# Optimization experiments

Hardware: AMD Instinct MI355X
Metric: run time of the kernel (lower is better)

## Reference

```python
import jax, jax.numpy as jnp
import numpy as np

D, H, W = 256, 256, 256
R = 6                      # max_radius: per-Gaussian half-window in voxels


def setup_inputs() -> dict:
    key = jax.random.key(0)
    k1, k2, k3, k4, k5 = jax.random.split(key, 5)
    N = 20000
    center_vox = jax.random.uniform(k1, (N, 3), minval=float(R), maxval=float(D - R), dtype=jnp.float32)
    A = jax.random.normal(k2, (N, 3, 3), dtype=jnp.float32) * 0.5
    # SPD inverse covariance in normalized coords (diffs divided by half_shape ~128)
    cov_inv = (jnp.einsum('nij,nkj->nik', A, A) + jnp.eye(3, dtype=jnp.float32)) * 2000.0
    density_r = jax.random.normal(k3, (N,), dtype=jnp.float32)
    density_i = jax.random.normal(k4, (N,), dtype=jnp.float32)
    radius_vox = jax.random.uniform(k5, (N,), minval=3.0, maxval=float(R), dtype=jnp.float32)
    half_shape = jnp.array([D / 2.0, H / 2.0, W / 2.0], dtype=jnp.float32)
    return {
        'center_vox': center_vox,
        'cov_inv': cov_inv,
        'density_r': density_r,
        'density_i': density_i,
        'radius_vox': radius_vox,
        'half_shape': half_shape,
    }


def reference(center_vox, cov_inv, density_r, density_i, radius_vox, half_shape):
    # Per-Gaussian fixed window of side (2R+1); gather -> Mahalanobis weight -> scatter-add.
    offs = jnp.arange(-R, R + 1, dtype=jnp.int32)
    od, oh, ow = jnp.meshgrid(offs, offs, offs, indexing='ij')
    off = jnp.stack([od, oh, ow], axis=-1).reshape(-1, 3)          # [K3,3]
    base = jnp.floor(center_vox).astype(jnp.int32)                  # [N,3]
    vox = base[:, None, :] + off[None, :, :]                        # [N,K3,3] int
    voxf = vox.astype(center_vox.dtype)
    diff = (voxf - center_vox[:, None, :]) / half_shape             # normalized diff [N,K3,3]
    Md = jnp.einsum('nkd,nde,nke->nk', diff, cov_inv, diff)         # Mahalanobis [N,K3]
    # bbox mask (floor(c-r) .. ceil(c+r)) as in build_tile_pairs / CUDA kernel
    bmin = jnp.floor(center_vox - radius_vox[:, None])
    bmax = jnp.ceil(center_vox + radius_vox[:, None])
    in_bbox = jnp.all((voxf >= bmin[:, None, :]) & (voxf <= bmax[:, None, :]), axis=-1)
    dims = jnp.array([D, H, W], dtype=jnp.int32)
    in_grid = jnp.all((vox >= 0) & (vox < dims), axis=-1)
    mask = (Md <= 9.0) & in_bbox & in_grid
    w = jnp.exp(-0.5 * Md) * mask.astype(Md.dtype)                  # [N,K3]
    flat = jnp.where(in_grid, vox[..., 0] * (H * W) + vox[..., 1] * W + vox[..., 2], 0).reshape(-1)
    vol_r = jnp.zeros(D * H * W, dtype=w.dtype).at[flat].add((w * density_r[:, None]).reshape(-1))
    vol_i = jnp.zeros(D * H * W, dtype=w.dtype).at[flat].add((w * density_i[:, None]).reshape(-1))
    return vol_r.reshape(D, H, W), vol_i.reshape(D, H, W)
```

## Files before the change

kernel.cpp:

```cpp
#include <hip/hip_runtime.h>

#define DD 256
#define HH 256
#define WW 256
#define RMAX 6

#define NTX 64
#define NTY 64
#define NTZ 16
#define NTILES (NTX * NTY * NTZ)
#define CAP 32
#define OVF_CAP 8192

__global__ __launch_bounds__(256) void fill_kernel(
    const float* __restrict__ center, const float* __restrict__ cov_inv,
    const float* __restrict__ dens_r, const float* __restrict__ dens_i,
    const float* __restrict__ radius,
    int* __restrict__ tile_cnt, int* __restrict__ tile_list,
    int* __restrict__ ovf_cnt, int* __restrict__ ovf_list,
    float* __restrict__ packed, int N)
{
    int i = blockIdx.x * 256 + threadIdx.x;
    if (i >= N) return;
    float cx = center[3*i+0], cy = center[3*i+1], cz = center[3*i+2];
    float r  = radius[i];
    float c00=cov_inv[9*i+0], c01=cov_inv[9*i+1], c02=cov_inv[9*i+2];
    float c10=cov_inv[9*i+3], c11=cov_inv[9*i+4], c12=cov_inv[9*i+5];
    float c20=cov_inv[9*i+6], c21=cov_inv[9*i+7], c22=cov_inv[9*i+8];

    float* P = packed + 12*i;
    P[0]=cx; P[1]=cy; P[2]=cz;
    P[3]=c00; P[4]=c11; P[5]=c22;
    P[6]=c01+c10; P[7]=c02+c20; P[8]=c12+c21;
    P[9]=dens_r[i]; P[10]=dens_i[i]; P[11]=r;

    int bx=(int)floorf(cx), by=(int)floorf(cy), bz=(int)floorf(cz);
    int xlo = max(max((int)floorf(cx - r), bx - RMAX), 0);
    int xhi = min(min((int)ceilf (cx + r), bx + RMAX), DD - 1);
    int ylo = max(max((int)floorf(cy - r), by - RMAX), 0);
    int yhi = min(min((int)ceilf (cy + r), by + RMAX), HH - 1);
    int zlo = max(max((int)floorf(cz - r), bz - RMAX), 0);
    int zhi = min(min((int)ceilf (cz + r), bz + RMAX), WW - 1);
    if (xlo > xhi || ylo > yhi || zlo > zhi) return;

    for (int tx = xlo >> 2; tx <= (xhi >> 2); ++tx)
        for (int ty = ylo >> 2; ty <= (yhi >> 2); ++ty)
            for (int tz = zlo >> 4; tz <= (zhi >> 4); ++tz) {
                int tile = (tx << 10) | (ty << 4) | tz;
                int pos = atomicAdd(&tile_cnt[tile], 1);
                if (pos < CAP) {
                    tile_list[tile * CAP + pos] = i;
                } else {
                    int o = atomicAdd(ovf_cnt, 1);
                    if (o < OVF_CAP) { ovf_list[2*o] = tile; ovf_list[2*o+1] = i; }
                }
            }
}

__global__ __launch_bounds__(64) void gather_kernel(
    const int* __restrict__ tile_cnt, const int* __restrict__ tile_list,
    const float* __restrict__ packed, const float* __restrict__ half_shape,
    float* __restrict__ vol_r, float* __restrict__ vol_i)
{
    int tile = blockIdx.x;
    int tz = tile & 15, ty = (tile >> 4) & 63, tx = tile >> 10;
    int t = threadIdx.x;
    int dx = t >> 4, dy = (t >> 2) & 3, dzq = t & 3;
    int vx = tx*4 + dx, vy = ty*4 + dy, vz0 = tz*16 + dzq*4;
    float vxf = (float)vx, vyf = (float)vy;
    float ihx = 1.0f/half_shape[0], ihy = 1.0f/half_shape[1], ihz = 1.0f/half_shape[2];

    float accr[4] = {0.f,0.f,0.f,0.f};
    float acci[4] = {0.f,0.f,0.f,0.f};

    int n = min(tile_cnt[tile], CAP);
    for (int j = 0; j < n; ++j) {
        int g = __builtin_amdgcn_readfirstlane(tile_list[tile * CAP + j]);
        const float* P = packed + 12*g;
        float cx=P[0], cy=P[1], cz=P[2];
        float s00=P[3], s11=P[4], s22=P[5];
        float s01=P[6], s02=P[7], s12=P[8];
        float dr=P[9], di=P[10], r=P[11];

        int bxi=(int)floorf(cx), byi=(int)floorf(cy), bzi=(int)floorf(cz);
        int xlo = max(max((int)floorf(cx - r), bxi - RMAX), 0);
        int xhi = min(min((int)ceilf (cx + r), bxi + RMAX), DD - 1);
        int ylo = max(max((int)floorf(cy - r), byi - RMAX), 0);
        int yhi = min(min((int)ceilf (cy + r), byi + RMAX), HH - 1);
        int zlo = max(max((int)floorf(cz - r), bzi - RMAX), 0);
        int zhi = min(min((int)ceilf (cz + r), bzi + RMAX), WW - 1);

        bool okxy = (vx >= xlo) && (vx <= xhi) && (vy >= ylo) && (vy <= yhi);
        float fx = (vxf - cx) * ihx;
        float fy = (vyf - cy) * ihy;
        float axy = s00*fx*fx + s01*fx*fy + s11*fy*fy;
        float bxy = s02*fx + s12*fy;

        #pragma unroll
        for (int k = 0; k < 4; ++k) {
            int vz = vz0 + k;
            float fz = ((float)vz - cz) * ihz;
            float md = axy + fz*(bxy + s22*fz);
            bool ok = okxy && (vz >= zlo) && (vz <= zhi) && (md <= 9.0f);
            if (ok) {
                float w = __expf(-0.5f * md);
                accr[k] += w * dr;
                acci[k] += w * di;
            }
        }
    }

    size_t flat = ((size_t)vx * HH + vy) * WW + vz0;
    *(float4*)(vol_r + flat) = make_float4(accr[0], accr[1], accr[2], accr[3]);
    *(float4*)(vol_i + flat) = make_float4(acci[0], acci[1], acci[2], acci[3]);
}

__global__ __launch_bounds__(256) void ovf_kernel(
    const int* __restrict__ ovf_cnt, const int* __restrict__ ovf_list,
    const float* __restrict__ packed, const float* __restrict__ half_shape,
    float* __restrict__ vol_r, float* __restrict__ vol_i)
{
    int total = min(ovf_cnt[0], OVF_CAP);
    if (total == 0) return;
    float ihx = 1.0f/half_shape[0], ihy = 1.0f/half_shape[1], ihz = 1.0f/half_shape[2];
    long work = (long)total * 64;
    for (long idx = (long)blockIdx.x * blockDim.x + threadIdx.x; idx < work;
         idx += (long)gridDim.x * blockDim.x) {
        int p = (int)(idx >> 6), lane = (int)(idx & 63);
        int tile = ovf_list[2*p], g = ovf_list[2*p+1];
        int tz = tile & 15, ty = (tile >> 4) & 63, tx = tile >> 10;
        int dx = lane >> 4, dy = (lane >> 2) & 3, dzq = lane & 3;
        int vx = tx*4 + dx, vy = ty*4 + dy, vz0 = tz*16 + dzq*4;

        const float* P = packed + 12*g;
        float cx=P[0], cy=P[1], cz=P[2];
        float s00=P[3], s11=P[4], s22=P[5];
        float s01=P[6], s02=P[7], s12=P[8];
        float dr=P[9], di=P[10], r=P[11];

        int bxi=(int)floorf(cx), byi=(int)floorf(cy), bzi=(int)floorf(cz);
        int xlo = max(max((int)floorf(cx - r), bxi - RMAX), 0);
        int xhi = min(min((int)ceilf (cx + r), bxi + RMAX), DD - 1);
        int ylo = max(max((int)floorf(cy - r), byi - RMAX), 0);
        int yhi = min(min((int)ceilf (cy + r), byi + RMAX), HH - 1);
        int zlo = max(max((int)floorf(cz - r), bzi - RMAX), 0);
        int zhi = min(min((int)ceilf (cz + r), bzi + RMAX), WW - 1);

        if ((vx < xlo) || (vx > xhi) || (vy < ylo) || (vy > yhi)) continue;
        float fx = ((float)vx - cx) * ihx;
        float fy = ((float)vy - cy) * ihy;
        float axy = s00*fx*fx + s01*fx*fy + s11*fy*fy;
        float bxy = s02*fx + s12*fy;
        for (int k = 0; k < 4; ++k) {
            int vz = vz0 + k;
            float fz = ((float)vz - cz) * ihz;
            float md = axy + fz*(bxy + s22*fz);
            if ((vz >= zlo) && (vz <= zhi) && (md <= 9.0f)) {
                float w = __expf(-0.5f * md);
                size_t flat = ((size_t)vx * HH + vy) * WW + vz;
                atomicAdd(&vol_r[flat], w * dr);
                atomicAdd(&vol_i[flat], w * di);
            }
        }
    }
}

__global__ __launch_bounds__(256) void splat_kernel(
    const float* __restrict__ center, const float* __restrict__ cov_inv,
    const float* __restrict__ dens_r, const float* __restrict__ dens_i,
    const float* __restrict__ radius, const float* __restrict__ half_shape,
    float* __restrict__ vol_r, float* __restrict__ vol_i, int N)
{
    int g = blockIdx.x;
    if (g >= N) return;
    float cx = center[3*g+0], cy = center[3*g+1], cz = center[3*g+2];
    float r  = radius[g];
    float c00 = cov_inv[9*g+0], c01 = cov_inv[9*g+1], c02 = cov_inv[9*g+2];
    float c10 = cov_inv[9*g+3], c11 = cov_inv[9*g+4], c12 = cov_inv[9*g+5];
    float c20 = cov_inv[9*g+6], c21 = cov_inv[9*g+7], c22 = cov_inv[9*g+8];
    float dr = dens_r[g], di = dens_i[g];
    float ihx = 1.0f/half_shape[0], ihy = 1.0f/half_shape[1], ihz = 1.0f/half_shape[2];
    int bx = (int)floorf(cx), by = (int)floorf(cy), bz = (int)floorf(cz);
    int xlo = max(max((int)floorf(cx - r), bx - RMAX), 0);
    int xhi = min(min((int)ceilf (cx + r), bx + RMAX), DD - 1);
    int ylo = max(max((int)floorf(cy - r), by - RMAX), 0);
    int yhi = min(min((int)ceilf (cy + r), by + RMAX), HH - 1);
    int zlo = max(max((int)floorf(cz - r), bz - RMAX), 0);
    int zhi = min(min((int)ceilf (cz + r), bz + RMAX), WW - 1);
    int nx = xhi-xlo+1, ny = yhi-ylo+1, nz = zhi-zlo+1;
    if (nx <= 0 || ny <= 0 || nz <= 0) return;
    int total = nx*ny*nz;
    for (int k = threadIdx.x; k < total; k += 256) {
        int iz = k % nz, tq = k / nz, iy = tq % ny, ix = tq / ny;
        int vx = xlo+ix, vy = ylo+iy, vz = zlo+iz;
        float dxn = ((float)vx - cx) * ihx;
        float dyn = ((float)vy - cy) * ihy;
        float dzn = ((float)vz - cz) * ihz;
        float md = dxn*(c00*dxn + c01*dyn + c02*dzn)
                 + dyn*(c10*dxn + c11*dyn + c12*dzn)
                 + dzn*(c20*dxn + c21*dyn + c22*dzn);
        if (md <= 9.0f) {
            float w = __expf(-0.5f*md);
            int flat = (vx*HH + vy)*WW + vz;
            atomicAdd(&vol_r[flat], w*dr);
            atomicAdd(&vol_i[flat], w*di);
        }
    }
}

extern "C" void kernel_launch(void* const* d_in, const int* in_sizes, int n_in,
                              void* d_out, int out_size, void* d_ws, size_t ws_size,
                              hipStream_t stream) {
    const float* center     = (const float*)d_in[0];
    const float* cov_inv    = (const float*)d_in[1];
    const float* dens_r     = (const float*)d_in[2];
    const float* dens_i     = (const float*)d_in[3];
    const float* radius     = (const float*)d_in[4];
    const float* half_shape = (const float*)d_in[5];
    int N = in_sizes[0] / 3;

    float* vol_r = (float*)d_out;
    float* vol_i = vol_r + (size_t)DD * HH * WW;

    size_t need = ((size_t)NTILES + 4 + 2*OVF_CAP + (size_t)NTILES*CAP) * sizeof(int)
                  + (size_t)N * 12 * sizeof(float);
    if (ws_size < need) {
        (void)hipMemsetAsync(d_out, 0, (size_t)out_size * sizeof(float), stream);
        splat_kernel<<<N, 256, 0, stream>>>(center, cov_inv, dens_r, dens_i,
                                            radius, half_shape, vol_r, vol_i, N);
        return;
    }

    int* tile_cnt  = (int*)d_ws;
    int* ovf_cnt   = tile_cnt + NTILES;
    int* ovf_list  = ovf_cnt + 4;
    int* tile_list = ovf_list + 2*OVF_CAP;
    float* packed  = (float*)(tile_list + (size_t)NTILES * CAP);

    (void)hipMemsetAsync(tile_cnt, 0, ((size_t)NTILES + 4) * sizeof(int), stream);
    fill_kernel<<<(N + 255)/256, 256, 0, stream>>>(center, cov_inv, dens_r, dens_i,
                                                   radius, tile_cnt, tile_list,
                                                   ovf_cnt, ovf_list, packed, N);
    gather_kernel<<<NTILES, 64, 0, stream>>>(tile_cnt, tile_list, packed, half_shape,
                                             vol_r, vol_i);
    ovf_kernel<<<64, 256, 0, stream>>>(ovf_cnt, ovf_list, packed, half_shape,
                                       vol_r, vol_i);
}
```

Baseline: 221.2 us.

## Store full Gaussian records per tile, tighten bboxes by ellipsoid extent, stage in LDS

The fill kernel now writes a 64-byte record per tile entry, holding center, symmetric cov terms, densities and the packed integer bbox. This replaces the index list plus indirect packed fetch. Bboxes are tightened by the analytic extent of the md<=9 ellipsoid, which cuts tile entries and overflow. The gather kernel processes four tiles per 256-thread block, stages the records in LDS, computes z-slices with FMAs, and skips exp work when no lane in the wave qualifies. The costs are much larger workspace and write traffic, a smaller per-tile capacity (24), and the ovf kernel now reads raw inputs with the untightened bbox.

```diff
diff --git a/kernel.cpp b/kernel.cpp
--- a/kernel.cpp
+++ b/kernel.cpp
@@ -5,43 +5,51 @@
 #define WW 256
 #define RMAX 6
 
-#define NTX 64
-#define NTY 64
-#define NTZ 16
-#define NTILES (NTX * NTY * NTZ)
-#define CAP 32
+#define NTILES 65536
+#define CAP 24
+#define RECSZ 16
 #define OVF_CAP 8192
 
 __global__ __launch_bounds__(256) void fill_kernel(
     const float* __restrict__ center, const float* __restrict__ cov_inv,
     const float* __restrict__ dens_r, const float* __restrict__ dens_i,
-    const float* __restrict__ radius,
-    int* __restrict__ tile_cnt, int* __restrict__ tile_list,
-    int* __restrict__ ovf_cnt, int* __restrict__ ovf_list,
-    float* __restrict__ packed, int N)
+    const float* __restrict__ radius, const float* __restrict__ half_shape,
+    int* __restrict__ tile_cnt, float* __restrict__ tile_recs,
+    int* __restrict__ ovf_cnt, int* __restrict__ ovf_list, int N)
 {
     int i = blockIdx.x * 256 + threadIdx.x;
     if (i >= N) return;
     float cx = center[3*i+0], cy = center[3*i+1], cz = center[3*i+2];
     float r  = radius[i];
     float c00=cov_inv[9*i+0], c01=cov_inv[9*i+1], c02=cov_inv[9*i+2];
-    float c10=cov_inv[9*i+3], c11=cov_inv[9*i+4], c12=cov_inv[9*i+5];
-    float c20=cov_inv[9*i+6], c21=cov_inv[9*i+7], c22=cov_inv[9*i+8];
-
-    float* P = packed + 12*i;
-    P[0]=cx; P[1]=cy; P[2]=cz;
-    P[3]=c00; P[4]=c11; P[5]=c22;
-    P[6]=c01+c10; P[7]=c02+c20; P[8]=c12+c21;
-    P[9]=dens_r[i]; P[10]=dens_i[i]; P[11]=r;
+    float c11=cov_inv[9*i+4], c12=cov_inv[9*i+5], c22=cov_inv[9*i+8];
+
+    float d00 = c11*c22 - c12*c12;
+    float d11 = c00*c22 - c02*c02;
+    float d22 = c00*c11 - c01*c01;
+    float det = c00*d00 - c01*(c01*c22 - c02*c12) + c02*(c01*c12 - c02*c11);
+    float k9  = 9.0f / det;
+    float hx = half_shape[0], hy = half_shape[1], hz = half_shape[2];
+    float ex = hx * sqrtf(d00 * k9) * 1.0001f + 0.01f;
+    float ey = hy * sqrtf(d11 * k9) * 1.0001f + 0.01f;
+    float ez = hz * sqrtf(d22 * k9) * 1.0001f + 0.01f;
+    float rx = fminf(r, ex), ry = fminf(r, ey), rz = fminf(r, ez);
 
     int bx=(int)floorf(cx), by=(int)floorf(cy), bz=(int)floorf(cz);
-    int xlo = max(max((int)floorf(cx - r), bx - RMAX), 0);
-    int xhi = min(min((int)ceilf (cx + r), bx + RMAX), DD - 1);
-    int ylo = max(max((int)floorf(cy - r), by - RMAX), 0);
-    int yhi = min(min((int)ceilf (cy + r), by + RMAX), HH - 1);
-    int zlo = max(max((int)floorf(cz - r), bz - RMAX), 0);
-    int zhi = min(min((int)ceilf (cz + r), bz + RMAX), WW - 1);
+    int xlo = max(max((int)floorf(cx - rx), bx - RMAX), 0);
+    int xhi = min(min((int)ceilf (cx + rx), bx + RMAX), DD - 1);
+    int ylo = max(max((int)floorf(cy - ry), by - RMAX), 0);
+    int yhi = min(min((int)ceilf (cy + ry), by + RMAX), HH - 1);
+    int zlo = max(max((int)floorf(cz - rz), bz - RMAX), 0);
+    int zhi = min(min((int)ceilf (cz + rz), bz + RMAX), WW - 1);
     if (xlo > xhi || ylo > yhi || zlo > zhi) return;
+
+    unsigned lo = (unsigned)xlo | ((unsigned)ylo << 8) | ((unsigned)zlo << 16);
+    unsigned hi = (unsigned)xhi | ((unsigned)yhi << 8) | ((unsigned)zhi << 16);
+    float4 r0 = make_float4(cx, cy, cz, c00);
+    float4 r1 = make_float4(c11, c22, c01 + c01, c02 + c02);
+    float4 r2 = make_float4(c12 + c12, dens_r[i], dens_i[i], __uint_as_float(lo));
+    float4 r3 = make_float4(__uint_as_float(hi), 0.f, 0.f, 0.f);
 
     for (int tx = xlo >> 2; tx <= (xhi >> 2); ++tx)
         for (int ty = ylo >> 2; ty <= (yhi >> 2); ++ty)
@@ -49,7 +57,8 @@
                 int tile = (tx << 10) | (ty << 4) | tz;
                 int pos = atomicAdd(&tile_cnt[tile], 1);
                 if (pos < CAP) {
-                    tile_list[tile * CAP + pos] = i;
+                    float4* R = (float4*)(tile_recs + ((size_t)tile * CAP + pos) * RECSZ);
+                    R[0] = r0; R[1] = r1; R[2] = r2; R[3] = r3;
                 } else {
                     int o = atomicAdd(ovf_cnt, 1);
                     if (o < OVF_CAP) { ovf_list[2*o] = tile; ovf_list[2*o+1] = i; }
@@ -57,109 +66,124 @@
             }
 }
 
-__global__ __launch_bounds__(64) void gather_kernel(
-    const int* __restrict__ tile_cnt, const int* __restrict__ tile_list,
-    const float* __restrict__ packed, const float* __restrict__ half_shape,
+__global__ __launch_bounds__(256) void gather_kernel(
+    const int* __restrict__ tile_cnt, const float* __restrict__ tile_recs,
+    const float* __restrict__ half_shape,
     float* __restrict__ vol_r, float* __restrict__ vol_i)
 {
-    int tile = blockIdx.x;
+    __shared__ float4 lds[4 * CAP * 4];
+    int w = threadIdx.x >> 6, lane = threadIdx.x & 63;
+    int tile = (blockIdx.x << 2) | w;
     int tz = tile & 15, ty = (tile >> 4) & 63, tx = tile >> 10;
-    int t = threadIdx.x;
-    int dx = t >> 4, dy = (t >> 2) & 3, dzq = t & 3;
-    int vx = tx*4 + dx, vy = ty*4 + dy, vz0 = tz*16 + dzq*4;
-    float vxf = (float)vx, vyf = (float)vy;
+    int dxl = lane >> 4, dyl = (lane >> 2) & 3, dzq = lane & 3;
+    int vx = tx*4 + dxl, vy = ty*4 + dyl, vz0 = tz*16 + dzq*4;
+    float vxf = (float)vx, vyf = (float)vy, vz0f = (float)vz0;
     float ihx = 1.0f/half_shape[0], ihy = 1.0f/half_shape[1], ihz = 1.0f/half_shape[2];
 
-    float accr[4] = {0.f,0.f,0.f,0.f};
-    float acci[4] = {0.f,0.f,0.f,0.f};
-
     int n = min(tile_cnt[tile], CAP);
+    float4* wl = lds + w * (CAP * 4);
+    const float4* src = (const float4*)(tile_recs + (size_t)tile * CAP * RECSZ);
+    for (int idx = lane; idx < n * 4; idx += 64) wl[idx] = src[idx];
+    __syncthreads();
+
+    float ar0=0.f, ar1=0.f, ar2=0.f, ar3=0.f;
+    float ai0=0.f, ai1=0.f, ai2=0.f, ai3=0.f;
+
     for (int j = 0; j < n; ++j) {
-        int g = __builtin_amdgcn_readfirstlane(tile_list[tile * CAP + j]);
-        const float* P = packed + 12*g;
-        float cx=P[0], cy=P[1], cz=P[2];
-        float s00=P[3], s11=P[4], s22=P[5];
-        float s01=P[6], s02=P[7], s12=P[8];
-        float dr=P[9], di=P[10], r=P[11];
-
-        int bxi=(int)floorf(cx), byi=(int)floorf(cy), bzi=(int)floorf(cz);
-        int xlo = max(max((int)floorf(cx - r), bxi - RMAX), 0);
-        int xhi = min(min((int)ceilf (cx + r), bxi + RMAX), DD - 1);
-        int ylo = max(max((int)floorf(cy - r), byi - RMAX), 0);
-        int yhi = min(min((int)ceilf (cy + r), byi + RMAX), HH - 1);
-        int zlo = max(max((int)floorf(cz - r), bzi - RMAX), 0);
-        int zhi = min(min((int)ceilf (cz + r), bzi + RMAX), WW - 1);
-
-        bool okxy = (vx >= xlo) && (vx <= xhi) && (vy >= ylo) && (vy <= yhi);
+        float4 r0 = wl[j*4+0];
+        float4 r1 = wl[j*4+1];
+        float4 r2 = wl[j*4+2];
+        float4 r3 = wl[j*4+3];
+        float cx=r0.x, cy=r0.y, cz=r0.z, s00=r0.w;
+        float s11=r1.x, s22=r1.y, s01=r1.z, s02=r1.w;
+        float s12=r2.x, dr=r2.y, di=r2.z;
+        unsigned lo = __float_as_uint(r2.w), hi = __float_as_uint(r3.x);
+        int xlo = lo & 255, ylo = (lo >> 8) & 255, zlo = (lo >> 16) & 255;
+        int xhi = hi & 255, yhi = (hi >> 8) & 255, zhi = (hi >> 16) & 255;
+
+        bool okxy = (vx >= xlo) & (vx <= xhi) & (vy >= ylo) & (vy <= yhi);
         float fx = (vxf - cx) * ihx;
         float fy = (vyf - cy) * ihy;
-        float axy = s00*fx*fx + s01*fx*fy + s11*fy*fy;
-        float bxy = s02*fx + s12*fy;
-
-        #pragma unroll
+        float axy = fx*fx*s00 + fx*fy*s01 + fy*fy*s11;
+        float bxy = fx*s02 + fy*s12;
+        float nczihz = -cz * ihz;
+
+        float fz0 = fmaf(vz0f, ihz, nczihz);
+        float fz1 = fz0 + ihz;
+        float fz2 = fz1 + ihz;
+        float fz3 = fz2 + ihz;
+        float md0 = fmaf(fz0, fmaf(s22, fz0, bxy), axy);
+        float md1 = fmaf(fz1, fmaf(s22, fz1, bxy), axy);
+        float md2 = fmaf(fz2, fmaf(s22, fz2, bxy), axy);
+        float md3 = fmaf(fz3, fmaf(s22, fz3, bxy), axy);
+
+        bool ok0 = okxy & (vz0   >= zlo) & (vz0   <= zhi) & (md0 <= 9.0f);
+        bool ok1 = okxy & (vz0+1 >= zlo) & (vz0+1 <= zhi) & (md1 <= 9.0f);
+        bool ok2 = okxy & (vz0+2 >= zlo) & (vz0+2 <= zhi) & (md2 <= 9.0f);
+        bool ok3 = okxy & (vz0+3 >= zlo) & (vz0+3 <= zhi) & (md3 <= 9.0f);
+
+        if (__any(ok0 | ok1 | ok2 | ok3)) {
+            float w0 = ok0 ? __expf(md0 * -0.5f) : 0.0f;
+            float w1 = ok1 ? __expf(md1 * -0.5f) : 0.0f;
+            float w2 = ok2 ? __expf(md2 * -0.5f) : 0.0f;
+            float w3 = ok3 ? __expf(md3 * -0.5f) : 0.0f;
+            ar0 = fmaf(w0, dr, ar0); ai0 = fmaf(w0, di, ai0);
+            ar1 = fmaf(w1, dr, ar1); ai1 = fmaf(w1, di, ai1);
+            ar2 = fmaf(w2, dr, ar2); ai2 = fmaf(w2, di, ai2);
+            ar3 = fmaf(w3, dr, ar3); ai3 = fmaf(w3, di, ai3);
+        }
+    }
+
+    size_t flat = ((size_t)vx * HH + vy) * WW + vz0;
+    *(float4*)(vol_r + flat) = make_float4(ar0, ar1, ar2, ar3);
+    *(float4*)(vol_i + flat) = make_float4(ai0, ai1, ai2, ai3);
+}
+
+__global__ __launch_bounds__(64) void ovf_kernel(
+    const int* __restrict__ ovf_cnt, const int* __restrict__ ovf_list,
+    const float* __restrict__ center, const float* __restrict__ cov_inv,
+    const float* __restrict__ dens_r, const float* __restrict__ dens_i,
+    const float* __restrict__ radius, const float* __restrict__ half_shape,
+    float* __restrict__ vol_r, float* __restrict__ vol_i)
+{
+    int total = min(ovf_cnt[0], OVF_CAP);
+    float ihx = 1.0f/half_shape[0], ihy = 1.0f/half_shape[1], ihz = 1.0f/half_shape[2];
+    int lane = threadIdx.x;
+    for (int p = blockIdx.x; p < total; p += gridDim.x) {
+        int tile = ovf_list[2*p], g = ovf_list[2*p+1];
+        int tz = tile & 15, ty = (tile >> 4) & 63, tx = tile >> 10;
+        int dxl = lane >> 4, dyl = (lane >> 2) & 3, dzq = lane & 3;
+        int vx = tx*4 + dxl, vy = ty*4 + dyl, vz0 = tz*16 + dzq*4;
+
+        float cx = center[3*g+0], cy = center[3*g+1], cz = center[3*g+2];
+        float r  = radius[g];
+        float c00=cov_inv[9*g+0], c01=cov_inv[9*g+1], c02=cov_inv[9*g+2];
+        float c10=cov_inv[9*g+3], c11=cov_inv[9*g+4], c12=cov_inv[9*g+5];
+        float c20=cov_inv[9*g+6], c21=cov_inv[9*g+7], c22=cov_inv[9*g+8];
+        float dr = dens_r[g], di = dens_i[g];
+
+        int bx=(int)floorf(cx), by=(int)floorf(cy), bz=(int)floorf(cz);
+        int xlo = max(max((int)floorf(cx - r), bx - RMAX), 0);
+        int xhi = min(min((int)ceilf (cx + r), bx + RMAX), DD - 1);
+        int ylo = max(max((int)floorf(cy - r), by - RMAX), 0);
+        int yhi = min(min((int)ceilf (cy + r), by + RMAX), HH - 1);
+        int zlo = max(max((int)floorf(cz - r), bz - RMAX), 0);
+        int zhi = min(min((int)ceilf (cz + r), bz + RMAX), WW - 1);
+
+        if (vx < xlo || vx > xhi || vy < ylo || vy > yhi) continue;
+        float fx = ((float)vx - cx) * ihx;
+        float fy = ((float)vy - cy) * ihy;
         for (int k = 0; k < 4; ++k) {
             int vz = vz0 + k;
             float fz = ((float)vz - cz) * ihz;
-            float md = axy + fz*(bxy + s22*fz);
-            bool ok = okxy && (vz >= zlo) && (vz <= zhi) && (md <= 9.0f);
-            if (ok) {
-                float w = __expf(-0.5f * md);
-                accr[k] += w * dr;
-                acci[k] += w * di;
-            }
-        }
-    }
-
-    size_t flat = ((size_t)vx * HH + vy) * WW + vz0;
-    *(float4*)(vol_r + flat) = make_float4(accr[0], accr[1], accr[2], accr[3]);
-    *(float4*)(vol_i + flat) = make_float4(acci[0], acci[1], acci[2], acci[3]);
-}
-
-__global__ __launch_bounds__(256) void ovf_kernel(
-    const int* __restrict__ ovf_cnt, const int* __restrict__ ovf_list,
-    const float* __restrict__ packed, const float* __restrict__ half_shape,
-    float* __restrict__ vol_r, float* __restrict__ vol_i)
-{
-    int total = min(ovf_cnt[0], OVF_CAP);
-    if (total == 0) return;
-    float ihx = 1.0f/half_shape[0], ihy = 1.0f/half_shape[1], ihz = 1.0f/half_shape[2];
-    long work = (long)total * 64;
-    for (long idx = (long)blockIdx.x * blockDim.x + threadIdx.x; idx < work;
-         idx += (long)gridDim.x * blockDim.x) {
-        int p = (int)(idx >> 6), lane = (int)(idx & 63);
-        int tile = ovf_list[2*p], g = ovf_list[2*p+1];
-        int tz = tile & 15, ty = (tile >> 4) & 63, tx = tile >> 10;
-        int dx = lane >> 4, dy = (lane >> 2) & 3, dzq = lane & 3;
-        int vx = tx*4 + dx, vy = ty*4 + dy, vz0 = tz*16 + dzq*4;
-
-        const float* P = packed + 12*g;
-        float cx=P[0], cy=P[1], cz=P[2];
-        float s00=P[3], s11=P[4], s22=P[5];
-        float s01=P[6], s02=P[7], s12=P[8];
-        float dr=P[9], di=P[10], r=P[11];
-
-        int bxi=(int)floorf(cx), byi=(int)floorf(cy), bzi=(int)floorf(cz);
-        int xlo = max(max((int)floorf(cx - r), bxi - RMAX), 0);
-        int xhi = min(min((int)ceilf (cx + r), bxi + RMAX), DD - 1);
-        int ylo = max(max((int)floorf(cy - r), byi - RMAX), 0);
-        int yhi = min(min((int)ceilf (cy + r), byi + RMAX), HH - 1);
-        int zlo = max(max((int)floorf(cz - r), bzi - RMAX), 0);
-        int zhi = min(min((int)ceilf (cz + r), bzi + RMAX), WW - 1);
-
-        if ((vx < xlo) || (vx > xhi) || (vy < ylo) || (vy > yhi)) continue;
-        float fx = ((float)vx - cx) * ihx;
-        float fy = ((float)vy - cy) * ihy;
-        float axy = s00*fx*fx + s01*fx*fy + s11*fy*fy;
-        float bxy = s02*fx + s12*fy;
-        for (int k = 0; k < 4; ++k) {
-            int vz = vz0 + k;
-            float fz = ((float)vz - cz) * ihz;
-            float md = axy + fz*(bxy + s22*fz);
-            if ((vz >= zlo) && (vz <= zhi) && (md <= 9.0f)) {
-                float w = __expf(-0.5f * md);
+            float md = fx*(c00*fx + c01*fy + c02*fz)
+                     + fy*(c10*fx + c11*fy + c12*fz)
+                     + fz*(c20*fx + c21*fy + c22*fz);
+            if (vz >= zlo && vz <= zhi && md <= 9.0f) {
+                float wgt = __expf(-0.5f * md);
                 size_t flat = ((size_t)vx * HH + vy) * WW + vz;
-                atomicAdd(&vol_r[flat], w * dr);
-                atomicAdd(&vol_i[flat], w * di);
+                atomicAdd(&vol_r[flat], wgt * dr);
+                atomicAdd(&vol_i[flat], wgt * di);
             }
         }
     }
@@ -200,10 +224,10 @@
                  + dyn*(c10*dxn + c11*dyn + c12*dzn)
                  + dzn*(c20*dxn + c21*dyn + c22*dzn);
         if (md <= 9.0f) {
-            float w = __expf(-0.5f*md);
+            float wgt = __expf(-0.5f*md);
             int flat = (vx*HH + vy)*WW + vz;
-            atomicAdd(&vol_r[flat], w*dr);
-            atomicAdd(&vol_i[flat], w*di);
+            atomicAdd(&vol_r[flat], wgt*dr);
+            atomicAdd(&vol_i[flat], wgt*di);
         }
     }
 }
@@ -222,8 +246,9 @@
     float* vol_r = (float*)d_out;
     float* vol_i = vol_r + (size_t)DD * HH * WW;
 
-    size_t need = ((size_t)NTILES + 4 + 2*OVF_CAP + (size_t)NTILES*CAP) * sizeof(int)
-                  + (size_t)N * 12 * sizeof(float);
+    size_t rec_floats = (size_t)NTILES * CAP * RECSZ;
+    size_t need = rec_floats * sizeof(float)
+                + ((size_t)NTILES + 4 + 2*OVF_CAP) * sizeof(int);
     if (ws_size < need) {
         (void)hipMemsetAsync(d_out, 0, (size_t)out_size * sizeof(float), stream);
         splat_kernel<<<N, 256, 0, stream>>>(center, cov_inv, dens_r, dens_i,
@@ -231,18 +256,19 @@
         return;
     }
 
-    int* tile_cnt  = (int*)d_ws;
-    int* ovf_cnt   = tile_cnt + NTILES;
-    int* ovf_list  = ovf_cnt + 4;
-    int* tile_list = ovf_list + 2*OVF_CAP;
-    float* packed  = (float*)(tile_list + (size_t)NTILES * CAP);
+    float* tile_recs = (float*)d_ws;
+    int*   tile_cnt  = (int*)(tile_recs + rec_floats);
+    int*   ovf_cnt   = tile_cnt + NTILES;
+    int*   ovf_list  = ovf_cnt + 4;
 
     (void)hipMemsetAsync(tile_cnt, 0, ((size_t)NTILES + 4) * sizeof(int), stream);
     fill_kernel<<<(N + 255)/256, 256, 0, stream>>>(center, cov_inv, dens_r, dens_i,
-                                                   radius, tile_cnt, tile_list,
-                                                   ovf_cnt, ovf_list, packed, N);
-    gather_kernel<<<NTILES, 64, 0, stream>>>(tile_cnt, tile_list, packed, half_shape,
-                                             vol_r, vol_i);
-    ovf_kernel<<<64, 256, 0, stream>>>(ovf_cnt, ovf_list, packed, half_shape,
-                                       vol_r, vol_i);
-}
+                                                   radius, half_shape,
+                                                   tile_cnt, tile_recs,
+                                                   ovf_cnt, ovf_list, N);
+    gather_kernel<<<NTILES/4, 256, 0, stream>>>(tile_cnt, tile_recs, half_shape,
+                                                vol_r, vol_i);
+    ovf_kernel<<<64, 64, 0, stream>>>(ovf_cnt, ovf_list, center, cov_inv,
+                                      dens_r, dens_i, radius, half_shape,
+                                      vol_r, vol_i);
+}
```

Measured after the change: 219.7 us. No clear change (-0.7%).
